# Kernel tuning notes

Measured on AMD Instinct MI355X. Metric: run time of the kernel, lower is better.

Reference implementation:

```python
import jax, jax.numpy as jnp
import numpy as np

N = 100_000
E = 3_200_000
F_IN = 512
F_OUT = 256
ALPHA = 0.2      # LeakyReLU negative slope
EPS = 9e-15      # matches torch.Tensor([9e-15]) in the original


def setup_inputs() -> dict:
    key = jax.random.key(0)
    k_x, k_e, k_w, k_a, k_b = jax.random.split(key, 5)
    x = jax.random.normal(k_x, (N, F_IN), dtype=jnp.float32)
    edge = jax.random.randint(k_e, (2, E), 0, N, dtype=jnp.int64)
    # xavier_normal-ish scales
    W = jax.random.normal(k_w, (F_IN, F_OUT), dtype=jnp.float32) * (1.414 * np.sqrt(2.0 / (F_IN + F_OUT)))
    a = jax.random.normal(k_a, (2 * F_OUT,), dtype=jnp.float32) * (1.414 * np.sqrt(2.0 / (1 + 2 * F_OUT)))
    bias = jax.random.normal(k_b, (F_OUT,), dtype=jnp.float32) * (1.414 * np.sqrt(2.0 / (1 + F_OUT)))
    return {"x": x, "edge": edge, "W": W, "a": a, "bias": bias}


def reference(x, edge, W, a, bias):
    src, dst = edge[0], edge[1]
    n = x.shape[0]
    h = x @ W + bias  # [N, F_OUT]
    # a . cat(h[src], h[dst]) == (h @ a_src)[src] + (h @ a_dst)[dst]
    a_src, a_dst = a[:F_OUT], a[F_OUT:]
    e = (h @ a_src)[src] + (h @ a_dst)[dst]            # [E]
    e = jnp.where(e > 0, e, ALPHA * e)                  # LeakyReLU
    e = jnp.exp(e - jnp.max(e))                         # global-max stabilized exp
    rowsum = jax.ops.segment_sum(e, src, num_segments=n)               # [N]
    h_prime = jax.ops.segment_sum(e[:, None] * h[dst], src, num_segments=n)  # [N, F_OUT]
    h_prime = h_prime / (rowsum[:, None] + EPS)
    return jax.nn.elu(h_prime)
```

## Files before the change

### kernel.cpp

```cpp
#include <hip/hip_runtime.h>

typedef __bf16 bf16x8 __attribute__((ext_vector_type(8)));
typedef float f32x4 __attribute__((ext_vector_type(4)));
typedef unsigned short u16x8 __attribute__((ext_vector_type(8)));

#define FIN 512
#define FOUT 256
#define NBLK 256
#define BSHIFT 8

__device__ __forceinline__ float b2f(unsigned short u) {
  union { unsigned int u; float f; } x;
  x.u = ((unsigned int)u) << 16;
  return x.f;
}
__device__ __forceinline__ unsigned short f2b(float f) {
  union { float f; unsigned int u; } x; x.f = f;
  unsigned int u = x.u;
  unsigned int r = (u + 0x7fffu + ((u >> 16) & 1u)) >> 16;
  return (unsigned short)r;
}

__global__ void k_probe(const unsigned short* __restrict__ xh,
                        const int* __restrict__ e, int* __restrict__ flags) {
  __shared__ int cnt[2];
  if (threadIdx.x == 0) { cnt[0] = 0; cnt[1] = 0; }
  __syncthreads();
  int c = 0;
  for (int i = threadIdx.x; i < 32768; i += 256) {
    unsigned short u = xh[i];
    if (((u >> 7) & 0xFF) == 0xFF) c++;
  }
  if (c) atomicAdd(&cnt[0], c);
  if (e[2 * threadIdx.x + 1] == 0) atomicAdd(&cnt[1], 1);
  __syncthreads();
  if (threadIdx.x == 0) {
    flags[0] = (cnt[0] > 0) ? 1 : 0;
    flags[1] = (cnt[1] > 128) ? 1 : 0;
  }
}

__global__ void k_transpose(const void* __restrict__ W,
                            unsigned short* __restrict__ Wt,
                            const int* __restrict__ flags) {
  int idx = blockIdx.x * 256 + threadIdx.x;
  int k = idx >> 8, n = idx & 255;
  float v = flags[0] ? ((const float*)W)[idx]
                     : b2f(((const unsigned short*)W)[idx]);
  Wt[n * FIN + k] = f2b(v);
}

__global__ __launch_bounds__(256) void k_gemm(const void* __restrict__ X,
                                              const unsigned short* __restrict__ Wt,
                                              const void* __restrict__ bias,
                                              unsigned short* __restrict__ H,
                                              int nrows, const int* __restrict__ flags) {
  __shared__ char lds[65536];
  const int tid = threadIdx.x;
  const int wave = tid >> 6;
  const int lane = tid & 63;
  const int fm = lane & 15;
  const int fq = lane >> 4;
  const int isf = flags[0];
  const int m0 = blockIdx.x * 64;

  if (isf) {
#pragma unroll 4
    for (int j = 0; j < 16; ++j) {
      int r = wave * 16 + j;
      int grow = m0 + r; if (grow >= nrows) grow = nrows - 1;
      int c = lane ^ (j & 7);
      const float* gp = (const float*)X + (size_t)grow * FIN + c * 8;
      f32x4 lo = *(const f32x4*)gp;
      f32x4 hi = *(const f32x4*)(gp + 4);
      union { bf16x8 v; unsigned short u[8]; } cv;
#pragma unroll
      for (int k = 0; k < 4; k++) { cv.u[k] = f2b(lo[k]); cv.u[4 + k] = f2b(hi[k]); }
      *(bf16x8*)(lds + r * 1024 + lane * 16) = cv.v;
    }
  } else {
#pragma unroll
    for (int j = 0; j < 16; ++j) {
      int r = wave * 16 + j;
      int grow = m0 + r; if (grow >= nrows) grow = nrows - 1;
      int c = lane ^ (j & 7);
      const unsigned short* gp = (const unsigned short*)X + (size_t)grow * FIN + c * 8;
      __builtin_amdgcn_global_load_lds(
          (const __attribute__((address_space(1))) void*)gp,
          (__attribute__((address_space(3))) void*)(lds + r * 1024), 16, 0, 0);
    }
  }
  __syncthreads();

  f32x4 acc[4][4];
#pragma unroll
  for (int i = 0; i < 4; i++)
#pragma unroll
    for (int j = 0; j < 4; j++) acc[i][j] = (f32x4){0.f, 0.f, 0.f, 0.f};

  const unsigned short* wp[4];
#pragma unroll
  for (int i = 0; i < 4; i++)
    wp[i] = Wt + (size_t)((wave * 4 + i) * 16 + fm) * FIN + fq * 8;

  const int swz = fm & 7;
  bf16x8 bcur[4];
#pragma unroll
  for (int i = 0; i < 4; i++) bcur[i] = *(const bf16x8*)(wp[i]);

  for (int it = 0; it < 16; ++it) {
    int itn = (it + 1 < 16) ? it + 1 : 15;
    bf16x8 bnext[4];
#pragma unroll
    for (int i = 0; i < 4; i++) bnext[i] = *(const bf16x8*)(wp[i] + itn * 32);
    bf16x8 af[4];
#pragma unroll
    for (int mt = 0; mt < 4; mt++) {
      int slot = (it * 4 + fq) ^ swz;
      af[mt] = *(const bf16x8*)(lds + (mt * 16 + fm) * 1024 + slot * 16);
    }
#pragma unroll
    for (int mt = 0; mt < 4; mt++)
#pragma unroll
      for (int i = 0; i < 4; i++)
        acc[mt][i] = __builtin_amdgcn_mfma_f32_16x16x32_bf16(af[mt], bcur[i], acc[mt][i], 0, 0, 0);
#pragma unroll
    for (int i = 0; i < 4; i++) bcur[i] = bnext[i];
  }

#pragma unroll
  for (int i = 0; i < 4; i++) {
    int col = (wave * 4 + i) * 16 + fm;
    float bv = isf ? ((const float*)bias)[col] : b2f(((const unsigned short*)bias)[col]);
#pragma unroll
    for (int mt = 0; mt < 4; mt++) {
#pragma unroll
      for (int r = 0; r < 4; r++) {
        int row = m0 + mt * 16 + fq * 4 + r;
        if (row < nrows) H[(size_t)row * FOUT + col] = f2b(acc[mt][i][r] + bv);
      }
    }
  }
}

__global__ __launch_bounds__(256) void k_scores(const unsigned short* __restrict__ H,
                                                const void* __restrict__ a,
                                                float* __restrict__ s1, float* __restrict__ s2,
                                                int n, const int* __restrict__ flags) {
  int wave = threadIdx.x >> 6, lane = threadIdx.x & 63;
  int row = blockIdx.x * 4 + wave;
  if (row >= n) return;
  const ushort4* hp = (const ushort4*)(H + (size_t)row * FOUT);
  ushort4 hv = hp[lane];
  float as0, as1, as2, as3, ad0, ad1, ad2, ad3;
  if (flags[0]) {
    const float* af = (const float*)a;
    f32x4 s = *(const f32x4*)(af + lane * 4);
    f32x4 d = *(const f32x4*)(af + FOUT + lane * 4);
    as0 = s[0]; as1 = s[1]; as2 = s[2]; as3 = s[3];
    ad0 = d[0]; ad1 = d[1]; ad2 = d[2]; ad3 = d[3];
  } else {
    const ushort4* ap = (const ushort4*)a;
    ushort4 s = ap[lane], d = ap[64 + lane];
    as0 = b2f(s.x); as1 = b2f(s.y); as2 = b2f(s.z); as3 = b2f(s.w);
    ad0 = b2f(d.x); ad1 = b2f(d.y); ad2 = b2f(d.z); ad3 = b2f(d.w);
  }
  float h0 = b2f(hv.x), h1 = b2f(hv.y), h2 = b2f(hv.z), h3 = b2f(hv.w);
  float p1 = h0 * as0 + h1 * as1 + h2 * as2 + h3 * as3;
  float p2 = h0 * ad0 + h1 * ad1 + h2 * ad2 + h3 * ad3;
#pragma unroll
  for (int off = 32; off >= 1; off >>= 1) {
    p1 += __shfl_down(p1, off, 64);
    p2 += __shfl_down(p2, off, 64);
  }
  if (lane == 0) { s1[row] = p1; s2[row] = p2; }
}


__global__ __launch_bounds__(256) void k_bcount(const int* __restrict__ e, int E, int chunk,
                                                int nbuck, int* __restrict__ C,
                                                const int* __restrict__ flags) {
  __shared__ int hist[512];
  int t = threadIdx.x, blk = blockIdx.x;
  for (int i = t; i < nbuck; i += 256) hist[i] = 0;
  __syncthreads();
  int lo = blk * chunk, hi = min(E, lo + chunk);
  bool i64 = flags[1] != 0;
  for (int i = lo + t; i < hi; i += 256) {
    int s = i64 ? ((const int2*)e)[i].x : e[i];
    atomicAdd(&hist[s >> BSHIFT], 1);
  }
  __syncthreads();
  for (int i = t; i < nbuck; i += 256) C[blk * nbuck + i] = hist[i];
}

__global__ __launch_bounds__(256) void k_bscanA(const int* __restrict__ C, int nbuck,
                                                int* __restrict__ O, int* __restrict__ btot) {
  int b = blockIdx.x, t = threadIdx.x;
  int lane = t & 63, w = t >> 6;
  int v = C[t * nbuck + b];
  int x = v;
#pragma unroll
  for (int off = 1; off < 64; off <<= 1) {
    int y = __shfl_up(x, off, 64);
    if (lane >= off) x += y;
  }
  __shared__ int ws[4];
  if (lane == 63) ws[w] = x;
  __syncthreads();
  int wbase = (w > 0 ? ws[0] : 0) + (w > 1 ? ws[1] : 0) + (w > 2 ? ws[2] : 0);
  O[t * nbuck + b] = x + wbase - v;
  if (t == 255) btot[b] = x + wbase;
}

__global__ __launch_bounds__(512) void k_bscanB(const int* __restrict__ btot, int nbuck,
                                                int* __restrict__ bbase,
                                                int* __restrict__ rowptr, int N) {
  __shared__ int sh[512];
  int t = threadIdx.x;
  int v = (t < nbuck) ? btot[t] : 0;
  sh[t] = v;
  __syncthreads();
  for (int off = 1; off < 512; off <<= 1) {
    int u = (t >= off) ? sh[t - off] : 0;
    __syncthreads();
    sh[t] += u;
    __syncthreads();
  }
  if (t < nbuck) bbase[t] = sh[t] - v;
  if (t == nbuck - 1) { bbase[nbuck] = sh[t]; rowptr[N] = sh[t]; }
}

__global__ __launch_bounds__(256) void k_bscatter(const int* __restrict__ e, int E, int chunk,
                                                  int nbuck, const int* __restrict__ O,
                                                  const int* __restrict__ bbase,
                                                  int* __restrict__ stage,
                                                  const int* __restrict__ flags) {
  __shared__ int cur[512];
  int t = threadIdx.x, blk = blockIdx.x;
  for (int i = t; i < nbuck; i += 256) cur[i] = bbase[i] + O[blk * nbuck + i];
  __syncthreads();
  int lo = blk * chunk, hi = min(E, lo + chunk);
  bool i64 = flags[1] != 0;
  for (int i = lo + t; i < hi; i += 256) {
    int s, d;
    if (i64) { s = ((const int2*)e)[i].x; d = ((const int2*)e)[(size_t)E + i].x; }
    else     { s = e[i];                  d = e[E + i]; }
    int pos = atomicAdd(&cur[s >> BSHIFT], 1);
    stage[pos] = ((s & 255) << 17) | d;
  }
}

__global__ __launch_bounds__(256) void k_fine(const int* __restrict__ stage,
                                              const int* __restrict__ bbase,
                                              int* __restrict__ rowptr,
                                              int* __restrict__ csrd, int N) {
  __shared__ int hist[256];
  __shared__ int cursor[256];
  __shared__ int ws[4];
  int b = blockIdx.x, t = threadIdx.x;
  int s0 = b << BSHIFT;
  int base = bbase[b], end = bbase[b + 1], cnt = end - base;
  hist[t] = 0;
  __syncthreads();
  for (int i = t; i < cnt; i += 256) atomicAdd(&hist[stage[base + i] >> 17], 1);
  __syncthreads();
  int v = hist[t];
  int lane = t & 63, w = t >> 6;
  int x = v;
#pragma unroll
  for (int off = 1; off < 64; off <<= 1) {
    int y = __shfl_up(x, off, 64);
    if (lane >= off) x += y;
  }
  if (lane == 63) ws[w] = x;
  __syncthreads();
  int wbase = (w > 0 ? ws[0] : 0) + (w > 1 ? ws[1] : 0) + (w > 2 ? ws[2] : 0);
  int excl = x + wbase - v;
  cursor[t] = base + excl;
  if (s0 + t < N) rowptr[s0 + t] = base + excl;
  __syncthreads();
  for (int i = t; i < cnt; i += 256) {
    int p = stage[base + i];
    int pos = atomicAdd(&cursor[p >> 17], 1);
    csrd[pos] = p & 0x1FFFF;
  }
}

__global__ __launch_bounds__(256) void k_gather(const unsigned short* __restrict__ H,
                                                const float* __restrict__ s1,
                                                const float* __restrict__ s2,
                                                const int* __restrict__ rowptr,
                                                const int* __restrict__ csrd,
                                                void* __restrict__ out, int n,
                                                const int* __restrict__ flags) {
  __shared__ int2 eds[4][64];
  int wave = threadIdx.x >> 6, lane = threadIdx.x & 63;
  int row = blockIdx.x * 4 + wave;
  if (row >= n) return;
  int half = lane >> 5;
  int hl = lane & 31;
  int beg = rowptr[row], end = rowptr[row + 1];
  float s1v = s1[row];
  const unsigned short* Hb = H + hl * 8;
  float ac[8];
#pragma unroll
  for (int k = 0; k < 8; k++) ac[k] = 0.f;
  float wsum = 0.f;

  for (int base = beg; base < end; base += 64) {
    int cnt = end - base; if (cnt > 64) cnt = 64;
    int d_pre = 0;
    float s_pre = -1e30f;
    if (lane < cnt) { d_pre = csrd[base + lane]; s_pre = s2[d_pre]; }
    eds[wave][lane] = make_int2(d_pre, __float_as_int(s_pre));

#pragma unroll 4
    for (int j = 0; j < cnt; j += 2) {
      int jj = j + half;
      int2 p = eds[wave][jj];
      int dd = p.x;
      float v = s1v + __int_as_float(p.y);
      v = v > 0.f ? v : 0.2f * v;
      float w = (jj < cnt) ? __expf(v) : 0.f;
      union { u16x8 v; unsigned short u[8]; } hv;
      hv.v = *(const u16x8*)(Hb + (size_t)dd * FOUT);
      wsum += w;
#pragma unroll
      for (int k = 0; k < 8; k++) ac[k] += w * b2f(hv.u[k]);
    }
  }

#pragma unroll
  for (int k = 0; k < 8; k++) ac[k] += __shfl_down(ac[k], 32, 64);
  wsum += __shfl_down(wsum, 32, 64);

  if (half == 0) {
    float inv = 1.f / (wsum + 9e-15f);
    float o[8];
#pragma unroll
    for (int k = 0; k < 8; k++) {
      float x = ac[k] * inv;
      o[k] = x > 0.f ? x : __expf(x) - 1.f;
    }
    if (flags[0]) {
      float* op = (float*)out + (size_t)row * FOUT + hl * 8;
      *(f32x4*)op = (f32x4){o[0], o[1], o[2], o[3]};
      *(f32x4*)(op + 4) = (f32x4){o[4], o[5], o[6], o[7]};
    } else {
      union { u16x8 v; unsigned short u[8]; } ov;
#pragma unroll
      for (int k = 0; k < 8; k++) ov.u[k] = f2b(o[k]);
      *(u16x8*)((unsigned short*)out + (size_t)row * FOUT + hl * 8) = ov.v;
    }
  }
}

extern "C" void kernel_launch(void* const* d_in, const int* in_sizes, int n_in,
                              void* d_out, int out_size, void* d_ws, size_t ws_size,
                              hipStream_t stream) {
  const void* X = d_in[0];
  const int* edge = (const int*)d_in[1];
  const void* W = d_in[2];
  const void* A = d_in[3];
  const void* B = d_in[4];
  int N_ = in_sizes[0] / FIN;
  int E_ = in_sizes[1] / 2;
  int nbuck = (N_ + 255) >> BSHIFT;
  int chunk = (E_ + NBLK - 1) / NBLK;

  char* p = (char*)d_ws;
  auto alloc = [&](size_t bytes) {
    char* r = p; p += (bytes + 255) & ~(size_t)255; return r;
  };
  int* flags = (int*)alloc(256);
  unsigned short* H  = (unsigned short*)alloc((size_t)N_ * FOUT * 2);
  unsigned short* Wt = (unsigned short*)alloc((size_t)FIN * FOUT * 2);
  float* s1   = (float*)alloc((size_t)N_ * 4);
  float* s2   = (float*)alloc((size_t)N_ * 4);
  int* rowptr = (int*)alloc((size_t)(N_ + 1) * 4);
  int* csrd   = (int*)alloc((size_t)E_ * 4);
  int* C      = (int*)alloc((size_t)NBLK * nbuck * 4);
  int* O      = (int*)alloc((size_t)NBLK * nbuck * 4);
  int* btot   = (int*)alloc((size_t)nbuck * 4);
  int* bbase  = (int*)alloc((size_t)(nbuck + 1) * 4);
  int* stage  = (int*)alloc((size_t)E_ * 4);

  k_probe<<<1, 256, 0, stream>>>((const unsigned short*)X, edge, flags);
  k_transpose<<<(FIN * FOUT) / 256, 256, 0, stream>>>(W, Wt, flags);
  k_gemm<<<(N_ + 63) / 64, 256, 0, stream>>>(X, Wt, B, H, N_, flags);
  k_scores<<<(N_ + 3) / 4, 256, 0, stream>>>(H, A, s1, s2, N_, flags);
  k_bcount<<<NBLK, 256, 0, stream>>>(edge, E_, chunk, nbuck, C, flags);
  k_bscanA<<<nbuck, 256, 0, stream>>>(C, nbuck, O, btot);
  k_bscanB<<<1, 512, 0, stream>>>(btot, nbuck, bbase, rowptr, N_);
  k_bscatter<<<NBLK, 256, 0, stream>>>(edge, E_, chunk, nbuck, O, bbase, stage, flags);
  k_fine<<<nbuck, 256, 0, stream>>>(stage, bbase, rowptr, csrd, N_);
  k_gather<<<(N_ + 3) / 4, 256, 0, stream>>>(H, s1, s2, rowptr, csrd,
                                             d_out, N_, flags);
}
```

Baseline: 752.0 us.

## Fuse attention score projection into GEMM epilogue and use packed bf16 convert

Computes the per-node s1/s2 attention projections inside the GEMM epilogue from fp32 accumulators, using a 16-lane xor shuffle reduction and an LDS cross-wave sum. This removes the separate k_scores launch and its re-read of H. It also replaces the manual fp32-to-bf16 rounding in the X staging loop with the packed v_cvt_pk_bf16_f32 instruction, and raises the gather loop unroll from 4 to 8. Scores are now taken from unrounded fp32 h rather than bf16 H, which slightly changes numerics, and the epilogue adds a block barrier plus more register pressure.

```diff
diff --git a/kernel.cpp b/kernel.cpp
--- a/kernel.cpp
+++ b/kernel.cpp
@@ -19,6 +19,11 @@
   unsigned int u = x.u;
   unsigned int r = (u + 0x7fffu + ((u >> 16) & 1u)) >> 16;
   return (unsigned short)r;
+}
+__device__ __forceinline__ unsigned int cvt_pk_bf16(float lo, float hi) {
+  unsigned int r;
+  asm("v_cvt_pk_bf16_f32 %0, %1, %2" : "=v"(r) : "v"(lo), "v"(hi));
+  return r;
 }
 
 __global__ void k_probe(const unsigned short* __restrict__ xh,
@@ -53,7 +58,10 @@
 __global__ __launch_bounds__(256) void k_gemm(const void* __restrict__ X,
                                               const unsigned short* __restrict__ Wt,
                                               const void* __restrict__ bias,
+                                              const void* __restrict__ A,
                                               unsigned short* __restrict__ H,
+                                              float* __restrict__ s1,
+                                              float* __restrict__ s2,
                                               int nrows, const int* __restrict__ flags) {
   __shared__ char lds[65536];
   const int tid = threadIdx.x;
@@ -73,10 +81,12 @@
       const float* gp = (const float*)X + (size_t)grow * FIN + c * 8;
       f32x4 lo = *(const f32x4*)gp;
       f32x4 hi = *(const f32x4*)(gp + 4);
-      union { bf16x8 v; unsigned short u[8]; } cv;
-#pragma unroll
-      for (int k = 0; k < 4; k++) { cv.u[k] = f2b(lo[k]); cv.u[4 + k] = f2b(hi[k]); }
-      *(bf16x8*)(lds + r * 1024 + lane * 16) = cv.v;
+      uint4 pk;
+      pk.x = cvt_pk_bf16(lo[0], lo[1]);
+      pk.y = cvt_pk_bf16(lo[2], lo[3]);
+      pk.z = cvt_pk_bf16(hi[0], hi[1]);
+      pk.w = cvt_pk_bf16(hi[2], hi[3]);
+      *(uint4*)(lds + r * 1024 + lane * 16) = pk;
     }
   } else {
 #pragma unroll
@@ -128,52 +138,58 @@
     for (int i = 0; i < 4; i++) bcur[i] = bnext[i];
   }
 
+  __syncthreads();
+  float* sc1 = (float*)lds;
+  float* sc2 = sc1 + 256;
+
+  float bvv[4], asv[4], adv[4];
 #pragma unroll
   for (int i = 0; i < 4; i++) {
     int col = (wave * 4 + i) * 16 + fm;
-    float bv = isf ? ((const float*)bias)[col] : b2f(((const unsigned short*)bias)[col]);
-#pragma unroll
-    for (int mt = 0; mt < 4; mt++) {
-#pragma unroll
-      for (int r = 0; r < 4; r++) {
-        int row = m0 + mt * 16 + fq * 4 + r;
-        if (row < nrows) H[(size_t)row * FOUT + col] = f2b(acc[mt][i][r] + bv);
+    if (isf) {
+      bvv[i] = ((const float*)bias)[col];
+      asv[i] = ((const float*)A)[col];
+      adv[i] = ((const float*)A)[FOUT + col];
+    } else {
+      bvv[i] = b2f(((const unsigned short*)bias)[col]);
+      asv[i] = b2f(((const unsigned short*)A)[col]);
+      adv[i] = b2f(((const unsigned short*)A)[FOUT + col]);
+    }
+  }
+
+#pragma unroll
+  for (int mt = 0; mt < 4; mt++) {
+#pragma unroll
+    for (int r = 0; r < 4; r++) {
+      int row = m0 + mt * 16 + fq * 4 + r;
+      float p1 = 0.f, p2 = 0.f;
+#pragma unroll
+      for (int i = 0; i < 4; i++) {
+        float h = acc[mt][i][r] + bvv[i];
+        if (row < nrows) H[(size_t)row * FOUT + (wave * 4 + i) * 16 + fm] = f2b(h);
+        p1 += h * asv[i];
+        p2 += h * adv[i];
       }
-    }
-  }
-}
-
-__global__ __launch_bounds__(256) void k_scores(const unsigned short* __restrict__ H,
-                                                const void* __restrict__ a,
-                                                float* __restrict__ s1, float* __restrict__ s2,
-                                                int n, const int* __restrict__ flags) {
-  int wave = threadIdx.x >> 6, lane = threadIdx.x & 63;
-  int row = blockIdx.x * 4 + wave;
-  if (row >= n) return;
-  const ushort4* hp = (const ushort4*)(H + (size_t)row * FOUT);
-  ushort4 hv = hp[lane];
-  float as0, as1, as2, as3, ad0, ad1, ad2, ad3;
-  if (flags[0]) {
-    const float* af = (const float*)a;
-    f32x4 s = *(const f32x4*)(af + lane * 4);
-    f32x4 d = *(const f32x4*)(af + FOUT + lane * 4);
-    as0 = s[0]; as1 = s[1]; as2 = s[2]; as3 = s[3];
-    ad0 = d[0]; ad1 = d[1]; ad2 = d[2]; ad3 = d[3];
-  } else {
-    const ushort4* ap = (const ushort4*)a;
-    ushort4 s = ap[lane], d = ap[64 + lane];
-    as0 = b2f(s.x); as1 = b2f(s.y); as2 = b2f(s.z); as3 = b2f(s.w);
-    ad0 = b2f(d.x); ad1 = b2f(d.y); ad2 = b2f(d.z); ad3 = b2f(d.w);
-  }
-  float h0 = b2f(hv.x), h1 = b2f(hv.y), h2 = b2f(hv.z), h3 = b2f(hv.w);
-  float p1 = h0 * as0 + h1 * as1 + h2 * as2 + h3 * as3;
-  float p2 = h0 * ad0 + h1 * ad1 + h2 * ad2 + h3 * ad3;
-#pragma unroll
-  for (int off = 32; off >= 1; off >>= 1) {
-    p1 += __shfl_down(p1, off, 64);
-    p2 += __shfl_down(p2, off, 64);
-  }
-  if (lane == 0) { s1[row] = p1; s2[row] = p2; }
+#pragma unroll
+      for (int off = 1; off < 16; off <<= 1) {
+        p1 += __shfl_xor(p1, off, 64);
+        p2 += __shfl_xor(p2, off, 64);
+      }
+      if (fm == 0) {
+        int rl = mt * 16 + fq * 4 + r;
+        sc1[wave * 64 + rl] = p1;
+        sc2[wave * 64 + rl] = p2;
+      }
+    }
+  }
+  __syncthreads();
+  if (tid < 64) {
+    int row = m0 + tid;
+    if (row < nrows) {
+      s1[row] = sc1[tid] + sc1[64 + tid] + sc1[128 + tid] + sc1[192 + tid];
+      s2[row] = sc2[tid] + sc2[64 + tid] + sc2[128 + tid] + sc2[192 + tid];
+    }
+  }
 }
 
 
@@ -315,7 +331,7 @@
     if (lane < cnt) { d_pre = csrd[base + lane]; s_pre = s2[d_pre]; }
     eds[wave][lane] = make_int2(d_pre, __float_as_int(s_pre));
 
-#pragma unroll 4
+#pragma unroll 8
     for (int j = 0; j < cnt; j += 2) {
       int jj = j + half;
       int2 p = eds[wave][jj];
@@ -388,8 +404,7 @@
 
   k_probe<<<1, 256, 0, stream>>>((const unsigned short*)X, edge, flags);
   k_transpose<<<(FIN * FOUT) / 256, 256, 0, stream>>>(W, Wt, flags);
-  k_gemm<<<(N_ + 63) / 64, 256, 0, stream>>>(X, Wt, B, H, N_, flags);
-  k_scores<<<(N_ + 3) / 4, 256, 0, stream>>>(H, A, s1, s2, N_, flags);
+  k_gemm<<<(N_ + 63) / 64, 256, 0, stream>>>(X, Wt, B, A, H, s1, s2, N_, flags);
   k_bcount<<<NBLK, 256, 0, stream>>>(edge, E_, chunk, nbuck, C, flags);
   k_bscanA<<<nbuck, 256, 0, stream>>>(C, nbuck, O, btot);
   k_bscanB<<<1, 512, 0, stream>>>(btot, nbuck, bbase, rowptr, N_);
```

Result: faster. 728.9 us (-3.1%).
